# Kernel tuning notes

Measured on AMD Instinct MI355X. Metric: run time of the kernel, lower is better.

Reference implementation:

```python
import jax, jax.numpy as jnp
import numpy as np

NL, DM, DS, DC, EX = 4, 1024, 16, 4, 2
DI = EX * DM          # 2048 inner dim
DTR = DM // 16        # 64 dt_rank
HID, OUT = 2048, 1000
B, L = 2, 1024
EPS = 1e-5

def _ln(x, w, b):
    m = jnp.mean(x, -1, keepdims=True)
    v = jnp.var(x, -1, keepdims=True)
    return (x - m) / jnp.sqrt(v + EPS) * w + b

def _silu(x):
    return x * jax.nn.sigmoid(x)

def _dwconv(x, w, b):
    # x: (B,L,C), w: (C,K) depthwise causal conv
    K = w.shape[1]
    xp = jnp.pad(x, ((0, 0), (K - 1, 0), (0, 0)))
    kern = jnp.transpose(w)[:, None, :]  # (K,1,C)
    y = jax.lax.conv_general_dilated(xp, kern, (1,), 'VALID',
                                     dimension_numbers=('NLC', 'LIO', 'NLC'),
                                     feature_group_count=x.shape[-1])
    return y + b

def _selective_scan(xs_, dt, Bm, Cm, A, Dv):
    # xs_, dt: (B,L,DI); Bm, Cm: (B,L,DS); A: (DI,DS); Dv: (DI,)
    def step(h, inp):
        x_t, dt_t, B_t, C_t = inp  # (B,DI),(B,DI),(B,DS),(B,DS)
        dA = jnp.exp(dt_t[..., None] * A)                       # (B,DI,DS)
        h = dA * h + dt_t[..., None] * B_t[:, None, :] * x_t[..., None]
        return h, jnp.einsum('bdn,bn->bd', h, C_t)
    h0 = jnp.zeros((xs_.shape[0], A.shape[0], A.shape[1]), xs_.dtype)
    seq = tuple(jnp.swapaxes(t, 0, 1) for t in (xs_, dt, Bm, Cm))
    _, ys = jax.lax.scan(step, h0, seq)
    return jnp.swapaxes(ys, 0, 1) + xs_ * Dv

def _mamba_block(x, ipw, cw, cb, xpw, dpw, dpb, Alog, Dv, opw):
    xz = jnp.einsum('bld,ed->ble', x, ipw)          # (B,L,2*DI)
    xs_, z = jnp.split(xz, 2, -1)
    xs_ = _silu(_dwconv(xs_, cw, cb))
    xdbl = jnp.einsum('bld,ed->ble', xs_, xpw)      # (B,L,DTR+2*DS)
    dt, Bm, Cm = jnp.split(xdbl, [DTR, DTR + DS], -1)
    dt = jax.nn.softplus(jnp.einsum('blr,dr->bld', dt, dpw) + dpb)
    A = -jnp.exp(Alog)
    y = _selective_scan(xs_, dt, Bm, Cm, A, Dv)
    y = y * _silu(z)
    return jnp.einsum('bld,ed->ble', y, opw)

def setup_inputs() -> dict:
    key = jax.random.key(0)
    ks = jax.random.split(key, 16)
    s = 0.02
    return {
        'x': jax.random.normal(ks[0], (B, L, DM), jnp.float32),
        'ln_w': jnp.ones((NL, DM)), 'ln_b': jnp.zeros((NL, DM)),
        'in_proj_w': jax.random.normal(ks[1], (NL, 2 * DI, DM)) * s,
        'conv_w': jax.random.normal(ks[2], (NL, DI, DC)) * s,
        'conv_b': jnp.zeros((NL, DI)),
        'x_proj_w': jax.random.normal(ks[3], (NL, DTR + 2 * DS, DI)) * s,
        'dt_proj_w': jax.random.normal(ks[4], (NL, DI, DTR)) * s,
        'dt_proj_b': jax.random.uniform(ks[5], (NL, DI), minval=-4.0, maxval=-2.0),
        'A_log': jnp.log(jnp.broadcast_to(jnp.arange(1, DS + 1, dtype=jnp.float32), (NL, DI, DS)) + 0.0),
        'Dv': jnp.ones((NL, DI)),
        'out_proj_w': jax.random.normal(ks[6], (NL, DM, DI)) * s,
        'fn_w': jnp.ones((DM,)), 'fn_b': jnp.zeros((DM,)),
        'h1_w': jax.random.normal(ks[7], (HID, DM)) * s, 'h1_b': jnp.zeros((HID,)),
        'hln_w': jnp.ones((HID,)), 'hln_b': jnp.zeros((HID,)),
        'h2_w': jax.random.normal(ks[8], (OUT, HID)) * s, 'h2_b': jnp.zeros((OUT,)),
    }

def reference(x, ln_w, ln_b, in_proj_w, conv_w, conv_b, x_proj_w, dt_proj_w,
              dt_proj_b, A_log, Dv, out_proj_w, fn_w, fn_b,
              h1_w, h1_b, hln_w, hln_b, h2_w, h2_b):
    for i in range(NL):
        res = x
        xn = _ln(x, ln_w[i], ln_b[i])
        x = _mamba_block(xn, in_proj_w[i], conv_w[i], conv_b[i], x_proj_w[i],
                         dt_proj_w[i], dt_proj_b[i], A_log[i], Dv[i], out_proj_w[i]) + res
    x = _ln(x, fn_w, fn_b)
    last = x[:, -1, :]                               # (B, DM)
    h = jax.nn.gelu(_ln(last @ h1_w.T + h1_b, hln_w, hln_b), approximate=False)
    return h @ h2_w.T + h2_b                         # (B, OUT)
```

## Files before the change

kernel.cpp:

```cpp
#include <hip/hip_runtime.h>

typedef unsigned short u16;
using short8 = __attribute__((ext_vector_type(8))) short;
using f32x4  = __attribute__((ext_vector_type(4))) float;

#define NLAYER 4
#define DMODEL 1024
#define DSTATE 16
#define DINNER 2048
#define DTRANK 64
#define SEQL   1024
#define NBATCH 2
#define MTOK   2048
#define NCH    64
#define CLEN   16

__device__ __forceinline__ u16 f2bf(float f) {
  union { float f; unsigned int u; } cv; cv.f = f;
  return (u16)((cv.u + 0x7FFFu + ((cv.u >> 16) & 1u)) >> 16);
}
__device__ __forceinline__ float bf2f(u16 v) {
  union { unsigned int u; float f; } cv; cv.u = ((unsigned int)v) << 16; return cv.f;
}

__global__ __launch_bounds__(256) void f32_to_bf16_k(const float* __restrict__ src,
                                                     u16* __restrict__ dst, int n) {
  int i4 = (blockIdx.x * 256 + threadIdx.x) * 4;
  if (i4 >= n) return;
  float4 v = *(const float4*)&src[i4];
  ushort4 o; o.x = f2bf(v.x); o.y = f2bf(v.y); o.z = f2bf(v.z); o.w = f2bf(v.w);
  *(ushort4*)&dst[i4] = o;
}

__global__ __launch_bounds__(256) void cvt_pad_xproj_k(const float* __restrict__ src,
                                                       u16* __restrict__ dst) {
  int i4 = (blockIdx.x * 256 + threadIdx.x) * 4;
  int row = i4 >> 11, col = i4 & 2047;
  float4 v = make_float4(0.f, 0.f, 0.f, 0.f);
  if (row < 96) v = *(const float4*)&src[row * 2048 + col];
  ushort4 o; o.x = f2bf(v.x); o.y = f2bf(v.y); o.z = f2bf(v.z); o.w = f2bf(v.w);
  *(ushort4*)&dst[i4] = o;
}

__global__ __launch_bounds__(256) void cvt_dtin_k(const float* __restrict__ xdbl,
                                                  u16* __restrict__ dtin) {
  int i4 = (blockIdx.x * 256 + threadIdx.x) * 4;
  int m = i4 >> 6, r = i4 & 63;
  float4 v = *(const float4*)&xdbl[m * 128 + r];
  ushort4 o; o.x = f2bf(v.x); o.y = f2bf(v.y); o.z = f2bf(v.z); o.w = f2bf(v.w);
  *(ushort4*)&dtin[i4] = o;
}

__global__ __launch_bounds__(256) void ln_to_bf16_k(const float* __restrict__ X,
    const float* __restrict__ w, const float* __restrict__ b, u16* __restrict__ out) {
  int row = blockIdx.x, tid = threadIdx.x;
  const float* x = X + (size_t)row * 1024;
  float4 v = ((const float4*)x)[tid];
  float s = v.x + v.y + v.z + v.w;
  float q = v.x*v.x + v.y*v.y + v.z*v.z + v.w*v.w;
  for (int o = 32; o; o >>= 1) { s += __shfl_down(s, o); q += __shfl_down(q, o); }
  __shared__ float sb[4], qb[4];
  int wv = tid >> 6, lane = tid & 63;
  if (lane == 0) { sb[wv] = s; qb[wv] = q; }
  __syncthreads();
  s = sb[0] + sb[1] + sb[2] + sb[3];
  q = qb[0] + qb[1] + qb[2] + qb[3];
  float mean = s * (1.f / 1024.f);
  float var  = q * (1.f / 1024.f) - mean * mean;
  float rstd = rsqrtf(var + 1e-5f);
  float4 wv4 = ((const float4*)w)[tid];
  float4 bv4 = ((const float4*)b)[tid];
  ushort4 o4;
  o4.x = f2bf((v.x - mean) * rstd * wv4.x + bv4.x);
  o4.y = f2bf((v.y - mean) * rstd * wv4.y + bv4.y);
  o4.z = f2bf((v.z - mean) * rstd * wv4.z + bv4.z);
  o4.w = f2bf((v.w - mean) * rstd * wv4.w + bv4.w);
  ((ushort4*)(out + (size_t)row * 1024))[tid] = o4;
}

__device__ __forceinline__ void stage_tile(const u16* G, int ld, int row0, int k0,
                                           u16* S, int tid) {
  int w = tid >> 6;
#pragma unroll
  for (int j = 0; j < 2; ++j) {
    int t = tid + j * 256;
    int r = t >> 2;
    int c = (t & 3) << 3;
    const u16* g = G + (size_t)(row0 + r) * ld + (k0 + c);
    u16* s = S + w * 512 + j * 2048;
    __builtin_amdgcn_global_load_lds((const __attribute__((address_space(1))) void*)g,
                                     (__attribute__((address_space(3))) void*)s,
                                     16, 0, 0);
  }
}

template<int EPI>
__global__ __launch_bounds__(256) void gemm_bt(const u16* __restrict__ A,
    const u16* __restrict__ Bw, float* __restrict__ C, const float* __restrict__ bias,
    int lda, int ldb, int ldc, int kchunk) {
  __shared__ u16 As[128 * 32];
  __shared__ u16 Bs[128 * 32];
  int tid = threadIdx.x;
  int bm = blockIdx.x, bn = blockIdx.y;
  int kb = blockIdx.z * kchunk, ke = kb + kchunk;
  int lane = tid & 63, w = tid >> 6;
  int wr = (w >> 1) * 64, wc = (w & 1) * 64;
  int fr = lane & 15;
  int kg = (lane >> 4) * 8;
  f32x4 acc[4][4] = {};
  for (int k0 = kb; k0 < ke; k0 += 32) {
    __syncthreads();
    stage_tile(A, lda, bm * 128, k0, As, tid);
    stage_tile(Bw, ldb, bn * 128, k0, Bs, tid);
    __syncthreads();
    short8 a[4], b[4];
#pragma unroll
    for (int mf = 0; mf < 4; ++mf)
      a[mf] = *(const short8*)&As[(wr + mf * 16 + fr) * 32 + kg];
#pragma unroll
    for (int nf = 0; nf < 4; ++nf)
      b[nf] = *(const short8*)&Bs[(wc + nf * 16 + fr) * 32 + kg];
#pragma unroll
    for (int mf = 0; mf < 4; ++mf)
#pragma unroll
      for (int nf = 0; nf < 4; ++nf)
        acc[mf][nf] = __builtin_amdgcn_mfma_f32_16x16x32_bf16(a[mf], b[nf], acc[mf][nf], 0, 0, 0);
  }
  int r0 = bm * 128 + wr + (lane >> 4) * 4;
  int c0 = bn * 128 + wc + (lane & 15);
#pragma unroll
  for (int mf = 0; mf < 4; ++mf) {
#pragma unroll
    for (int nf = 0; nf < 4; ++nf) {
#pragma unroll
      for (int r = 0; r < 4; ++r) {
        int gr = r0 + mf * 16 + r;
        int gc = c0 + nf * 16;
        float v = acc[mf][nf][r];
        size_t idx = (size_t)gr * ldc + gc;
        if (EPI == 0) {
          C[idx] = v;
        } else if (EPI == 1) {
          ((u16*)C)[idx] = f2bf(v);
        } else if (EPI == 2) {
          v += bias[gc];
          v = (v > 20.f) ? v : log1pf(__expf(v));
          C[idx] = v;
        } else {
          atomicAdd(&C[idx], v);
        }
      }
    }
  }
}

__global__ __launch_bounds__(256) void conv_silu_k(const u16* __restrict__ xzb,
    const float* __restrict__ cw, const float* __restrict__ cb,
    u16* __restrict__ xsb) {
  int idx = blockIdx.x * 256 + threadIdx.x;
  int m = idx >> 9;
  int d = (idx & 511) << 2;
  int t = m & (SEQL - 1);
  float4 w0 = *(const float4*)&cw[(d + 0) * 4];
  float4 w1 = *(const float4*)&cw[(d + 1) * 4];
  float4 w2 = *(const float4*)&cw[(d + 2) * 4];
  float4 w3 = *(const float4*)&cw[(d + 3) * 4];
  float4 acc = *(const float4*)&cb[d];
#pragma unroll
  for (int j = 0; j < 4; ++j) {
    int tt = t - 3 + j;
    if (tt >= 0) {
      ushort4 xv = *(const ushort4*)&xzb[(size_t)(m - 3 + j) * 4096 + d];
      acc.x += bf2f(xv.x) * ((const float*)&w0)[j];
      acc.y += bf2f(xv.y) * ((const float*)&w1)[j];
      acc.z += bf2f(xv.z) * ((const float*)&w2)[j];
      acc.w += bf2f(xv.w) * ((const float*)&w3)[j];
    }
  }
  float4 o;
  o.x = acc.x / (1.f + __expf(-acc.x));
  o.y = acc.y / (1.f + __expf(-acc.y));
  o.z = acc.z / (1.f + __expf(-acc.z));
  o.w = acc.w / (1.f + __expf(-acc.w));
  ushort4 ob; ob.x = f2bf(o.x); ob.y = f2bf(o.y); ob.z = f2bf(o.z); ob.w = f2bf(o.w);
  *(ushort4*)&xsb[(size_t)m * 2048 + d] = ob;
}


__global__ __launch_bounds__(256) void scan_part1(const float* __restrict__ dt,
    const u16* __restrict__ xsb, const float* __restrict__ xdbl,
    const float* __restrict__ Alog, float* __restrict__ PS) {
  int tid = threadIdx.x;
  int dg = blockIdx.x & 7;
  int ch = (blockIdx.x >> 3) & (NCH - 1);
  int b  = blockIdx.x >> 9;
  int d  = dg * 256 + tid;
  float Ar[16];
#pragma unroll
  for (int q = 0; q < 4; ++q) {
    float4 a = *(const float4*)&Alog[d * 16 + q * 4];
    Ar[q*4+0] = -__expf(a.x); Ar[q*4+1] = -__expf(a.y);
    Ar[q*4+2] = -__expf(a.z); Ar[q*4+3] = -__expf(a.w);
  }
  __shared__ float Bs[CLEN][16];
  if (tid < CLEN * 16) {
    int t = tid >> 4, n = tid & 15;
    int m = b * SEQL + ch * CLEN + t;
    Bs[t][n] = xdbl[m * 128 + 64 + n];
  }
  __syncthreads();
  int mbase = b * SEQL + ch * CLEN;
  float dtv[CLEN], xv[CLEN];
#pragma unroll
  for (int t = 0; t < CLEN; ++t) dtv[t] = dt[(size_t)(mbase + t) * 2048 + d];
#pragma unroll
  for (int t = 0; t < CLEN; ++t) xv[t] = bf2f(xsb[(size_t)(mbase + t) * 2048 + d]);
  float S[16];
#pragma unroll
  for (int n = 0; n < 16; ++n) S[n] = 0.f;
  float sumdt = 0.f;
  for (int t = 0; t < CLEN; ++t) {
    sumdt += dtv[t];
    float dx = dtv[t] * xv[t];
    float4 B0 = *(const float4*)&Bs[t][0];
    float4 B1 = *(const float4*)&Bs[t][4];
    float4 B2 = *(const float4*)&Bs[t][8];
    float4 B3 = *(const float4*)&Bs[t][12];
    const float* Bp[4] = {(const float*)&B0, (const float*)&B1, (const float*)&B2, (const float*)&B3};
#pragma unroll
    for (int n = 0; n < 16; ++n)
      S[n] = __expf(dtv[t] * Ar[n]) * S[n] + dx * Bp[n >> 2][n & 3];
  }
  float* p = PS + ((size_t)(b * NCH + ch) * 2048 + d) * 32;
#pragma unroll
  for (int n = 0; n < 16; ++n) p[n] = S[n];
#pragma unroll
  for (int n = 0; n < 16; ++n) p[16 + n] = __expf(Ar[n] * sumdt);
}

__global__ __launch_bounds__(256) void scan_prefix(const float* __restrict__ PS,
                                                   float* __restrict__ Hstart) {
  int id = blockIdx.x * 256 + threadIdx.x;
  int n = id & 15;
  int d = (id >> 4) & 2047;
  int b = id >> 15;
  size_t sbase = ((size_t)b * NCH) * 2048 * 32 + (size_t)d * 32 + n;
  size_t hbase = ((size_t)b * NCH) * 2048 * 16 + (size_t)d * 16 + n;
  float h = 0.f;
#pragma unroll 8
  for (int ch = 0; ch < NCH; ++ch) {
    Hstart[hbase + (size_t)ch * (2048 * 16)] = h;
    float S = PS[sbase + (size_t)ch * (2048 * 32)];
    float P = PS[sbase + (size_t)ch * (2048 * 32) + 16];
    h = fmaf(P, h, S);
  }
}

__global__ __launch_bounds__(256) void scan_part2(const float* __restrict__ dt,
    const u16* __restrict__ xsb, const float* __restrict__ xdbl,
    const float* __restrict__ Alog, const float* __restrict__ Dv,
    const u16* __restrict__ xzb, const float* __restrict__ Hstart,
    u16* __restrict__ yg) {
  int tid = threadIdx.x;
  int dg = blockIdx.x & 7;
  int ch = (blockIdx.x >> 3) & (NCH - 1);
  int b  = blockIdx.x >> 9;
  int d  = dg * 256 + tid;
  float Ar[16];
#pragma unroll
  for (int q = 0; q < 4; ++q) {
    float4 a = *(const float4*)&Alog[d * 16 + q * 4];
    Ar[q*4+0] = -__expf(a.x); Ar[q*4+1] = -__expf(a.y);
    Ar[q*4+2] = -__expf(a.z); Ar[q*4+3] = -__expf(a.w);
  }
  float Dvd = Dv[d];
  __shared__ float BCs[CLEN][32];
  if (tid < 256) {
    int t = tid >> 5, n = tid & 31;
    int m = b * SEQL + ch * CLEN + t;
    BCs[t][n] = xdbl[m * 128 + 64 + n];
    int t2 = t + 8;
    int m2 = m + 8;
    BCs[t2][n] = xdbl[m2 * 128 + 64 + n];
  }
  const float* hs = Hstart + ((size_t)(b * NCH + ch) * 2048 + d) * 16;
  float h[16];
#pragma unroll
  for (int q = 0; q < 4; ++q) {
    float4 hv = *(const float4*)&hs[q * 4];
    h[q*4+0] = hv.x; h[q*4+1] = hv.y; h[q*4+2] = hv.z; h[q*4+3] = hv.w;
  }
  int mbase = b * SEQL + ch * CLEN;
  float dtv[CLEN], xv[CLEN], zv[CLEN];
#pragma unroll
  for (int t = 0; t < CLEN; ++t) dtv[t] = dt[(size_t)(mbase + t) * 2048 + d];
#pragma unroll
  for (int t = 0; t < CLEN; ++t) xv[t] = bf2f(xsb[(size_t)(mbase + t) * 2048 + d]);
#pragma unroll
  for (int t = 0; t < CLEN; ++t) zv[t] = bf2f(xzb[(size_t)(mbase + t) * 4096 + 2048 + d]);
  __syncthreads();
  for (int t = 0; t < CLEN; ++t) {
    float dx = dtv[t] * xv[t];
    float4 B0 = *(const float4*)&BCs[t][0];
    float4 B1 = *(const float4*)&BCs[t][4];
    float4 B2 = *(const float4*)&BCs[t][8];
    float4 B3 = *(const float4*)&BCs[t][12];
    float4 C0 = *(const float4*)&BCs[t][16];
    float4 C1 = *(const float4*)&BCs[t][20];
    float4 C2 = *(const float4*)&BCs[t][24];
    float4 C3 = *(const float4*)&BCs[t][28];
    const float* Bp[4] = {(const float*)&B0, (const float*)&B1, (const float*)&B2, (const float*)&B3};
    const float* Cp[4] = {(const float*)&C0, (const float*)&C1, (const float*)&C2, (const float*)&C3};
#pragma unroll
    for (int n = 0; n < 16; ++n)
      h[n] = __expf(dtv[t] * Ar[n]) * h[n] + dx * Bp[n >> 2][n & 3];
    float y0 = 0.f, y1 = 0.f, y2 = 0.f, y3 = 0.f;
#pragma unroll
    for (int n = 0; n < 4; ++n) {
      y0 += h[n]      * Cp[0][n];
      y1 += h[4 + n]  * Cp[1][n];
      y2 += h[8 + n]  * Cp[2][n];
      y3 += h[12 + n] * Cp[3][n];
    }
    float y = (y0 + y1) + (y2 + y3) + xv[t] * Dvd;
    float sz = zv[t] / (1.f + __expf(-zv[t]));
    yg[(size_t)(mbase + t) * 2048 + d] = f2bf(y * sz);
  }
}

__global__ __launch_bounds__(256) void final_ln_last_k(const float* __restrict__ xb,
    const float* __restrict__ w, const float* __restrict__ b, float* __restrict__ out) {
  int bb = blockIdx.x, tid = threadIdx.x;
  const float* x = xb + (size_t)(bb * 1024 + 1023) * 1024;
  float4 v = ((const float4*)x)[tid];
  float s = v.x + v.y + v.z + v.w;
  float q = v.x*v.x + v.y*v.y + v.z*v.z + v.w*v.w;
  for (int o = 32; o; o >>= 1) { s += __shfl_down(s, o); q += __shfl_down(q, o); }
  __shared__ float sb[4], qb[4];
  int wv = tid >> 6, lane = tid & 63;
  if (lane == 0) { sb[wv] = s; qb[wv] = q; }
  __syncthreads();
  s = sb[0] + sb[1] + sb[2] + sb[3];
  q = qb[0] + qb[1] + qb[2] + qb[3];
  float mean = s * (1.f / 1024.f);
  float rstd = rsqrtf(q * (1.f / 1024.f) - mean * mean + 1e-5f);
  float4 wv4 = ((const float4*)w)[tid];
  float4 bv4 = ((const float4*)b)[tid];
  float4 o;
  o.x = (v.x - mean) * rstd * wv4.x + bv4.x;
  o.y = (v.y - mean) * rstd * wv4.y + bv4.y;
  o.z = (v.z - mean) * rstd * wv4.z + bv4.z;
  o.w = (v.w - mean) * rstd * wv4.w + bv4.w;
  ((float4*)(out + bb * 1024))[tid] = o;
}

__global__ __launch_bounds__(256) void gemv_head1_k(const float* __restrict__ X,
    const float* __restrict__ W, const float* __restrict__ bias, float* __restrict__ out) {
  int gw = (blockIdx.x * 256 + threadIdx.x) >> 6;
  int lane = threadIdx.x & 63;
  int b = gw >> 11, j = gw & 2047;
  const float* x = X + b * 1024;
  const float* w = W + (size_t)j * 1024;
  float s = 0.f;
#pragma unroll
  for (int q = 0; q < 4; ++q) {
    int col = q * 256 + lane * 4;
    float4 xv = *(const float4*)&x[col];
    float4 wv = *(const float4*)&w[col];
    s += xv.x*wv.x + xv.y*wv.y + xv.z*wv.z + xv.w*wv.w;
  }
  for (int o = 32; o; o >>= 1) s += __shfl_down(s, o);
  if (lane == 0) out[gw] = s + bias[j];
}

__global__ __launch_bounds__(256) void ln_gelu_k(const float* __restrict__ X,
    const float* __restrict__ w, const float* __restrict__ b, float* __restrict__ out) {
  int row = blockIdx.x, tid = threadIdx.x;
  const float* x = X + (size_t)row * 2048;
  float4 v0 = ((const float4*)x)[tid];
  float4 v1 = ((const float4*)x)[tid + 256];
  float s = v0.x+v0.y+v0.z+v0.w + v1.x+v1.y+v1.z+v1.w;
  float q = v0.x*v0.x+v0.y*v0.y+v0.z*v0.z+v0.w*v0.w
          + v1.x*v1.x+v1.y*v1.y+v1.z*v1.z+v1.w*v1.w;
  for (int o = 32; o; o >>= 1) { s += __shfl_down(s, o); q += __shfl_down(q, o); }
  __shared__ float sb[4], qb[4];
  int wv = tid >> 6, lane = tid & 63;
  if (lane == 0) { sb[wv] = s; qb[wv] = q; }
  __syncthreads();
  s = sb[0] + sb[1] + sb[2] + sb[3];
  q = qb[0] + qb[1] + qb[2] + qb[3];
  float mean = s * (1.f / 2048.f);
  float rstd = rsqrtf(q * (1.f / 2048.f) - mean * mean + 1e-5f);
  float* o0 = out + (size_t)row * 2048;
#pragma unroll
  for (int h = 0; h < 2; ++h) {
    float4 v = h ? v1 : v0;
    int c0 = tid * 4 + h * 1024;
    float4 wv4 = *(const float4*)&w[c0];
    float4 bv4 = *(const float4*)&b[c0];
    float4 g;
    g.x = (v.x - mean) * rstd * wv4.x + bv4.x;
    g.y = (v.y - mean) * rstd * wv4.y + bv4.y;
    g.z = (v.z - mean) * rstd * wv4.z + bv4.z;
    g.w = (v.w - mean) * rstd * wv4.w + bv4.w;
    g.x = 0.5f * g.x * (1.f + erff(g.x * 0.70710678f));
    g.y = 0.5f * g.y * (1.f + erff(g.y * 0.70710678f));
    g.z = 0.5f * g.z * (1.f + erff(g.z * 0.70710678f));
    g.w = 0.5f * g.w * (1.f + erff(g.w * 0.70710678f));
    *(float4*)&o0[c0] = g;
  }
}

__global__ __launch_bounds__(256) void gemv_head2_k(const float* __restrict__ X,
    const float* __restrict__ W, const float* __restrict__ bias, float* __restrict__ out) {
  int gw = (blockIdx.x * 256 + threadIdx.x) >> 6;
  int lane = threadIdx.x & 63;
  int b = (gw >= 1000) ? 1 : 0;
  int j = gw - b * 1000;
  const float* x = X + b * 2048;
  const float* w = W + (size_t)j * 2048;
  float s = 0.f;
#pragma unroll
  for (int q = 0; q < 8; ++q) {
    int col = q * 256 + lane * 4;
    float4 xv = *(const float4*)&x[col];
    float4 wv = *(const float4*)&w[col];
    s += xv.x*wv.x + xv.y*wv.y + xv.z*wv.z + xv.w*wv.w;
  }
  for (int o = 32; o; o >>= 1) s += __shfl_down(s, o);
  if (lane == 0) out[gw] = s + bias[j];
}

extern "C" void kernel_launch(void* const* d_in, const int* in_sizes, int n_in,
                              void* d_out, int out_size, void* d_ws, size_t ws_size,
                              hipStream_t stream) {
  const float* x_in = (const float*)d_in[0];
  const float* lnw  = (const float*)d_in[1];
  const float* lnb  = (const float*)d_in[2];
  const float* ipw  = (const float*)d_in[3];
  const float* cw   = (const float*)d_in[4];
  const float* cb   = (const float*)d_in[5];
  const float* xpw  = (const float*)d_in[6];
  const float* dpw  = (const float*)d_in[7];
  const float* dpb  = (const float*)d_in[8];
  const float* Alog = (const float*)d_in[9];
  const float* Dv   = (const float*)d_in[10];
  const float* opw  = (const float*)d_in[11];
  const float* fnw  = (const float*)d_in[12];
  const float* fnb  = (const float*)d_in[13];
  const float* h1w  = (const float*)d_in[14];
  const float* h1b  = (const float*)d_in[15];
  const float* hlnw = (const float*)d_in[16];
  const float* hlnb = (const float*)d_in[17];
  const float* h2w  = (const float*)d_in[18];
  const float* h2b  = (const float*)d_in[19];
  float* out = (float*)d_out;

  char* ws = (char*)d_ws;
  size_t off = 0;
  auto alloc = [&](size_t bytes) -> void* {
    void* p = ws + off; off += (bytes + 255) & ~(size_t)255; return p;
  };
  float* x_buf    = (float*)alloc((size_t)MTOK * DMODEL * 4);
  u16*   xn_bf    = (u16*)  alloc((size_t)MTOK * DMODEL * 2);
  u16*   xz_bf    = (u16*)  alloc((size_t)MTOK * 2 * DINNER * 2);
  u16*   xs_bf    = (u16*)  alloc((size_t)MTOK * DINNER * 2);
  float* xdbl     = (float*)alloc((size_t)MTOK * 128 * 4);
  u16*   dtin_bf  = (u16*)  alloc((size_t)MTOK * DTRANK * 2);
  float* dtbuf    = (float*)alloc((size_t)MTOK * DINNER * 4);
  u16*   yg_bf    = (u16*)  alloc((size_t)MTOK * DINNER * 2);
  u16*   w_ip     = (u16*)  alloc((size_t)2 * DINNER * DMODEL * 2);
  u16*   w_xp     = (u16*)  alloc((size_t)128 * DINNER * 2);
  u16*   w_dt     = (u16*)  alloc((size_t)DINNER * DTRANK * 2);
  u16*   w_op     = (u16*)  alloc((size_t)DMODEL * DINNER * 2);
  float* PS       = (float*)alloc((size_t)NBATCH * NCH * DINNER * 32 * 4);
  float* Hstart   = (float*)alloc((size_t)NBATCH * NCH * DINNER * 16 * 4);
  float* lastn    = (float*)alloc(2 * 1024 * 4);
  float* hpre     = (float*)alloc(2 * 2048 * 4);
  float* hbuf     = (float*)alloc(2 * 2048 * 4);

  hipMemcpyAsync(x_buf, x_in, (size_t)MTOK * DMODEL * 4, hipMemcpyDeviceToDevice, stream);

  for (int i = 0; i < NLAYER; ++i) {
    f32_to_bf16_k<<<4096, 256, 0, stream>>>(ipw + (size_t)i * 2 * DINNER * DMODEL, w_ip, 2 * DINNER * DMODEL);
    cvt_pad_xproj_k<<<256, 256, 0, stream>>>(xpw + (size_t)i * 96 * DINNER, w_xp);
    f32_to_bf16_k<<<128, 256, 0, stream>>>(dpw + (size_t)i * DINNER * DTRANK, w_dt, DINNER * DTRANK);
    f32_to_bf16_k<<<2048, 256, 0, stream>>>(opw + (size_t)i * DMODEL * DINNER, w_op, DMODEL * DINNER);
    ln_to_bf16_k<<<MTOK, 256, 0, stream>>>(x_buf, lnw + i * DMODEL, lnb + i * DMODEL, xn_bf);
    { dim3 g(16, 32, 1);
      gemm_bt<1><<<g, 256, 0, stream>>>(xn_bf, w_ip, (float*)xz_bf, nullptr, 1024, 1024, 4096, 1024); }
    conv_silu_k<<<4096, 256, 0, stream>>>(xz_bf, cw + (size_t)i * DINNER * 4, cb + i * DINNER, xs_bf);
    hipMemsetAsync(xdbl, 0, (size_t)MTOK * 128 * 4, stream);
    { dim3 g(16, 1, 8);
      gemm_bt<3><<<g, 256, 0, stream>>>(xs_bf, w_xp, xdbl, nullptr, 2048, 2048, 128, 256); }
    cvt_dtin_k<<<128, 256, 0, stream>>>(xdbl, dtin_bf);
    { dim3 g(16, 16, 1);
      gemm_bt<2><<<g, 256, 0, stream>>>(dtin_bf, w_dt, dtbuf, dpb + i * DINNER, 64, 64, 2048, 64); }
    scan_part1<<<1024, 256, 0, stream>>>(dtbuf, xs_bf, xdbl, Alog + (size_t)i * DINNER * DSTATE, PS);
    scan_prefix<<<256, 256, 0, stream>>>(PS, Hstart);
    scan_part2<<<1024, 256, 0, stream>>>(dtbuf, xs_bf, xdbl, Alog + (size_t)i * DINNER * DSTATE,
                                         Dv + i * DINNER, xz_bf, Hstart, yg_bf);
    { dim3 g(16, 8, 2);
      gemm_bt<3><<<g, 256, 0, stream>>>(yg_bf, w_op, x_buf, nullptr, 2048, 2048, 1024, 1024); }
  }
  final_ln_last_k<<<2, 256, 0, stream>>>(x_buf, fnw, fnb, lastn);
  gemv_head1_k<<<1024, 256, 0, stream>>>(lastn, h1w, h1b, hpre);
  ln_gelu_k<<<2, 256, 0, stream>>>(hpre, hlnw, hlnb, hbuf);
  gemv_head2_k<<<500, 256, 0, stream>>>(hbuf, h2w, h2b, out);
  (void)in_sizes; (void)n_in; (void)out_size; (void)ws_size;
}
```

Before: 800.0 us.

## Fuse conv into x_proj GEMM, double-buffer GEMM, batch weight conversion, bf16 dt

Weight conversion to bf16 now runs once for all layers in batched launches instead of four small launches per layer. The depthwise conv+SiLU is fused into the x_proj GEMM, which also writes xs. The dt-input conversion is fused into a dedicated dt GEMM that stores softplus(dt) as bf16, halving the dt traffic read by both scan kernels. The main GEMM gains LDS double buffering so the next tile loads while MFMA runs on the current one. The cost is more workspace, reduced dt precision, and redundant conv weight loads inside the fused kernel.

```diff
diff --git a/kernel.cpp b/kernel.cpp
--- a/kernel.cpp
+++ b/kernel.cpp
@@ -23,32 +23,25 @@
   union { unsigned int u; float f; } cv; cv.u = ((unsigned int)v) << 16; return cv.f;
 }
 
-__global__ __launch_bounds__(256) void f32_to_bf16_k(const float* __restrict__ src,
-                                                     u16* __restrict__ dst, int n) {
+__global__ __launch_bounds__(256) void f32_to_bf16_l(const float* __restrict__ src,
+                                                     u16* __restrict__ dst, int nper) {
+  int l = blockIdx.y;
   int i4 = (blockIdx.x * 256 + threadIdx.x) * 4;
-  if (i4 >= n) return;
-  float4 v = *(const float4*)&src[i4];
+  if (i4 >= nper) return;
+  float4 v = *(const float4*)&src[(size_t)l * nper + i4];
   ushort4 o; o.x = f2bf(v.x); o.y = f2bf(v.y); o.z = f2bf(v.z); o.w = f2bf(v.w);
-  *(ushort4*)&dst[i4] = o;
-}
-
-__global__ __launch_bounds__(256) void cvt_pad_xproj_k(const float* __restrict__ src,
+  *(ushort4*)&dst[(size_t)l * nper + i4] = o;
+}
+
+__global__ __launch_bounds__(256) void cvt_pad_xproj_l(const float* __restrict__ src,
                                                        u16* __restrict__ dst) {
+  int l = blockIdx.y;
   int i4 = (blockIdx.x * 256 + threadIdx.x) * 4;
   int row = i4 >> 11, col = i4 & 2047;
   float4 v = make_float4(0.f, 0.f, 0.f, 0.f);
-  if (row < 96) v = *(const float4*)&src[row * 2048 + col];
+  if (row < 96) v = *(const float4*)&src[(size_t)l * 96 * 2048 + row * 2048 + col];
   ushort4 o; o.x = f2bf(v.x); o.y = f2bf(v.y); o.z = f2bf(v.z); o.w = f2bf(v.w);
-  *(ushort4*)&dst[i4] = o;
-}
-
-__global__ __launch_bounds__(256) void cvt_dtin_k(const float* __restrict__ xdbl,
-                                                  u16* __restrict__ dtin) {
-  int i4 = (blockIdx.x * 256 + threadIdx.x) * 4;
-  int m = i4 >> 6, r = i4 & 63;
-  float4 v = *(const float4*)&xdbl[m * 128 + r];
-  ushort4 o; o.x = f2bf(v.x); o.y = f2bf(v.y); o.z = f2bf(v.z); o.w = f2bf(v.w);
-  *(ushort4*)&dtin[i4] = o;
+  *(ushort4*)&dst[(size_t)l * 128 * 2048 + i4] = o;
 }
 
 __global__ __launch_bounds__(256) void ln_to_bf16_k(const float* __restrict__ X,
@@ -96,10 +89,10 @@
 
 template<int EPI>
 __global__ __launch_bounds__(256) void gemm_bt(const u16* __restrict__ A,
-    const u16* __restrict__ Bw, float* __restrict__ C, const float* __restrict__ bias,
+    const u16* __restrict__ Bw, float* __restrict__ C,
     int lda, int ldb, int ldc, int kchunk) {
-  __shared__ u16 As[128 * 32];
-  __shared__ u16 Bs[128 * 32];
+  __shared__ u16 As[2][128 * 32];
+  __shared__ u16 Bs[2][128 * 32];
   int tid = threadIdx.x;
   int bm = blockIdx.x, bn = blockIdx.y;
   int kb = blockIdx.z * kchunk, ke = kb + kchunk;
@@ -108,26 +101,33 @@
   int fr = lane & 15;
   int kg = (lane >> 4) * 8;
   f32x4 acc[4][4] = {};
+  int cur = 0;
+  stage_tile(A, lda, bm * 128, kb, As[0], tid);
+  stage_tile(Bw, ldb, bn * 128, kb, Bs[0], tid);
+  __syncthreads();
   for (int k0 = kb; k0 < ke; k0 += 32) {
-    __syncthreads();
-    stage_tile(A, lda, bm * 128, k0, As, tid);
-    stage_tile(Bw, ldb, bn * 128, k0, Bs, tid);
-    __syncthreads();
+    int kn = k0 + 32;
+    if (kn < ke) {
+      stage_tile(A, lda, bm * 128, kn, As[cur ^ 1], tid);
+      stage_tile(Bw, ldb, bn * 128, kn, Bs[cur ^ 1], tid);
+    }
     short8 a[4], b[4];
 #pragma unroll
     for (int mf = 0; mf < 4; ++mf)
-      a[mf] = *(const short8*)&As[(wr + mf * 16 + fr) * 32 + kg];
+      a[mf] = *(const short8*)&As[cur][(wr + mf * 16 + fr) * 32 + kg];
 #pragma unroll
     for (int nf = 0; nf < 4; ++nf)
-      b[nf] = *(const short8*)&Bs[(wc + nf * 16 + fr) * 32 + kg];
+      b[nf] = *(const short8*)&Bs[cur][(wc + nf * 16 + fr) * 32 + kg];
 #pragma unroll
     for (int mf = 0; mf < 4; ++mf)
 #pragma unroll
       for (int nf = 0; nf < 4; ++nf)
         acc[mf][nf] = __builtin_amdgcn_mfma_f32_16x16x32_bf16(a[mf], b[nf], acc[mf][nf], 0, 0, 0);
+    __syncthreads();
+    cur ^= 1;
   }
   int r0 = bm * 128 + wr + (lane >> 4) * 4;
-  int c0 = bn * 128 + wc + (lane & 15);
+  int c0 = bn * 128 + wc + fr;
 #pragma unroll
   for (int mf = 0; mf < 4; ++mf) {
 #pragma unroll
@@ -138,14 +138,8 @@
         int gc = c0 + nf * 16;
         float v = acc[mf][nf][r];
         size_t idx = (size_t)gr * ldc + gc;
-        if (EPI == 0) {
-          C[idx] = v;
-        } else if (EPI == 1) {
+        if (EPI == 1) {
           ((u16*)C)[idx] = f2bf(v);
-        } else if (EPI == 2) {
-          v += bias[gc];
-          v = (v > 20.f) ? v : log1pf(__expf(v));
-          C[idx] = v;
         } else {
           atomicAdd(&C[idx], v);
         }
@@ -154,40 +148,151 @@
   }
 }
 
-__global__ __launch_bounds__(256) void conv_silu_k(const u16* __restrict__ xzb,
+__global__ __launch_bounds__(256) void xproj_conv_k(const u16* __restrict__ xzb,
     const float* __restrict__ cw, const float* __restrict__ cb,
-    u16* __restrict__ xsb) {
-  int idx = blockIdx.x * 256 + threadIdx.x;
-  int m = idx >> 9;
-  int d = (idx & 511) << 2;
-  int t = m & (SEQL - 1);
-  float4 w0 = *(const float4*)&cw[(d + 0) * 4];
-  float4 w1 = *(const float4*)&cw[(d + 1) * 4];
-  float4 w2 = *(const float4*)&cw[(d + 2) * 4];
-  float4 w3 = *(const float4*)&cw[(d + 3) * 4];
-  float4 acc = *(const float4*)&cb[d];
-#pragma unroll
-  for (int j = 0; j < 4; ++j) {
-    int tt = t - 3 + j;
-    if (tt >= 0) {
-      ushort4 xv = *(const ushort4*)&xzb[(size_t)(m - 3 + j) * 4096 + d];
-      acc.x += bf2f(xv.x) * ((const float*)&w0)[j];
-      acc.y += bf2f(xv.y) * ((const float*)&w1)[j];
-      acc.z += bf2f(xv.z) * ((const float*)&w2)[j];
-      acc.w += bf2f(xv.w) * ((const float*)&w3)[j];
+    const u16* __restrict__ Bw, u16* __restrict__ xsb, float* __restrict__ xdbl_l) {
+  __shared__ u16 As[128 * 32];
+  __shared__ u16 Bs[128 * 32];
+  int tid = threadIdx.x;
+  int bm = blockIdx.x;
+  int kb = blockIdx.z * 256;
+  int lane = tid & 63, w = tid >> 6;
+  int wr = (w >> 1) * 64, wc = (w & 1) * 64;
+  int fr = lane & 15;
+  int kg = (lane >> 4) * 8;
+  f32x4 acc[4][4] = {};
+  int r  = tid >> 1;
+  int cc = (tid & 1) * 16;
+  int m  = bm * 128 + r;
+  int tseq = m & (SEQL - 1);
+  for (int k0i = 0; k0i < 256; k0i += 32) {
+    int k0 = kb + k0i;
+    int d0 = k0 + cc;
+    float4 cw4[16];
+#pragma unroll
+    for (int i = 0; i < 16; ++i) cw4[i] = *(const float4*)&cw[(d0 + i) * 4];
+    float accv[16];
+#pragma unroll
+    for (int q = 0; q < 4; ++q) {
+      float4 c4 = *(const float4*)&cb[d0 + q * 4];
+      accv[q*4+0] = c4.x; accv[q*4+1] = c4.y; accv[q*4+2] = c4.z; accv[q*4+3] = c4.w;
     }
-  }
-  float4 o;
-  o.x = acc.x / (1.f + __expf(-acc.x));
-  o.y = acc.y / (1.f + __expf(-acc.y));
-  o.z = acc.z / (1.f + __expf(-acc.z));
-  o.w = acc.w / (1.f + __expf(-acc.w));
-  ushort4 ob; ob.x = f2bf(o.x); ob.y = f2bf(o.y); ob.z = f2bf(o.z); ob.w = f2bf(o.w);
-  *(ushort4*)&xsb[(size_t)m * 2048 + d] = ob;
-}
-
-
-__global__ __launch_bounds__(256) void scan_part1(const float* __restrict__ dt,
+#pragma unroll
+    for (int j = 0; j < 4; ++j) {
+      int tt = tseq - 3 + j;
+      if (tt >= 0) {
+        const u16* src = &xzb[(size_t)(m - 3 + j) * 4096 + d0];
+        short8 v0 = *(const short8*)src;
+        short8 v1 = *(const short8*)(src + 8);
+#pragma unroll
+        for (int i = 0; i < 8; ++i)
+          accv[i] += bf2f((u16)v0[i]) * ((const float*)&cw4[i])[j];
+#pragma unroll
+        for (int i = 0; i < 8; ++i)
+          accv[8 + i] += bf2f((u16)v1[i]) * ((const float*)&cw4[8 + i])[j];
+      }
+    }
+    short8 o0, o1;
+#pragma unroll
+    for (int i = 0; i < 8; ++i) {
+      float s0 = accv[i]     / (1.f + __expf(-accv[i]));
+      float s1 = accv[8 + i] / (1.f + __expf(-accv[8 + i]));
+      o0[i] = (short)f2bf(s0);
+      o1[i] = (short)f2bf(s1);
+    }
+    __syncthreads();
+    *(short8*)&As[r * 32 + cc]     = o0;
+    *(short8*)&As[r * 32 + cc + 8] = o1;
+    stage_tile(Bw, 2048, 0, k0, Bs, tid);
+    *(short8*)&xsb[(size_t)m * 2048 + d0]     = o0;
+    *(short8*)&xsb[(size_t)m * 2048 + d0 + 8] = o1;
+    __syncthreads();
+    short8 a[4], b[4];
+#pragma unroll
+    for (int mf = 0; mf < 4; ++mf)
+      a[mf] = *(const short8*)&As[(wr + mf * 16 + fr) * 32 + kg];
+#pragma unroll
+    for (int nf = 0; nf < 4; ++nf)
+      b[nf] = *(const short8*)&Bs[(wc + nf * 16 + fr) * 32 + kg];
+#pragma unroll
+    for (int mf = 0; mf < 4; ++mf)
+#pragma unroll
+      for (int nf = 0; nf < 4; ++nf)
+        acc[mf][nf] = __builtin_amdgcn_mfma_f32_16x16x32_bf16(a[mf], b[nf], acc[mf][nf], 0, 0, 0);
+  }
+  int r0 = bm * 128 + wr + (lane >> 4) * 4;
+  int c0 = wc + fr;
+#pragma unroll
+  for (int mf = 0; mf < 4; ++mf)
+#pragma unroll
+    for (int nf = 0; nf < 4; ++nf)
+#pragma unroll
+      for (int rr = 0; rr < 4; ++rr) {
+        int gr = r0 + mf * 16 + rr;
+        int gc = c0 + nf * 16;
+        atomicAdd(&xdbl_l[(size_t)gr * 128 + gc], acc[mf][nf][rr]);
+      }
+}
+
+__global__ __launch_bounds__(256) void gemm_dt_k(const float* __restrict__ Af,
+    const u16* __restrict__ Bw, const float* __restrict__ bias, u16* __restrict__ Cout) {
+  __shared__ u16 As[128 * 32];
+  __shared__ u16 Bs[128 * 32];
+  int tid = threadIdx.x;
+  int bm = blockIdx.x, bn = blockIdx.y;
+  int lane = tid & 63, w = tid >> 6;
+  int wr = (w >> 1) * 64, wc = (w & 1) * 64;
+  int fr = lane & 15;
+  int kg = (lane >> 4) * 8;
+  f32x4 acc[4][4] = {};
+  int r  = tid >> 1;
+  int cc = (tid & 1) * 16;
+  for (int k0 = 0; k0 < 64; k0 += 32) {
+    const float* src = &Af[(size_t)(bm * 128 + r) * 128 + k0 + cc];
+    float4 f0 = *(const float4*)&src[0];
+    float4 f1 = *(const float4*)&src[4];
+    float4 f2 = *(const float4*)&src[8];
+    float4 f3 = *(const float4*)&src[12];
+    short8 o0, o1;
+    o0[0]=(short)f2bf(f0.x); o0[1]=(short)f2bf(f0.y); o0[2]=(short)f2bf(f0.z); o0[3]=(short)f2bf(f0.w);
+    o0[4]=(short)f2bf(f1.x); o0[5]=(short)f2bf(f1.y); o0[6]=(short)f2bf(f1.z); o0[7]=(short)f2bf(f1.w);
+    o1[0]=(short)f2bf(f2.x); o1[1]=(short)f2bf(f2.y); o1[2]=(short)f2bf(f2.z); o1[3]=(short)f2bf(f2.w);
+    o1[4]=(short)f2bf(f3.x); o1[5]=(short)f2bf(f3.y); o1[6]=(short)f2bf(f3.z); o1[7]=(short)f2bf(f3.w);
+    __syncthreads();
+    *(short8*)&As[r * 32 + cc]     = o0;
+    *(short8*)&As[r * 32 + cc + 8] = o1;
+    stage_tile(Bw, 64, bn * 128, k0, Bs, tid);
+    __syncthreads();
+    short8 a[4], b[4];
+#pragma unroll
+    for (int mf = 0; mf < 4; ++mf)
+      a[mf] = *(const short8*)&As[(wr + mf * 16 + fr) * 32 + kg];
+#pragma unroll
+    for (int nf = 0; nf < 4; ++nf)
+      b[nf] = *(const short8*)&Bs[(wc + nf * 16 + fr) * 32 + kg];
+#pragma unroll
+    for (int mf = 0; mf < 4; ++mf)
+#pragma unroll
+      for (int nf = 0; nf < 4; ++nf)
+        acc[mf][nf] = __builtin_amdgcn_mfma_f32_16x16x32_bf16(a[mf], b[nf], acc[mf][nf], 0, 0, 0);
+  }
+  int r0 = bm * 128 + wr + (lane >> 4) * 4;
+  int c0 = bn * 128 + wc + fr;
+#pragma unroll
+  for (int mf = 0; mf < 4; ++mf)
+#pragma unroll
+    for (int nf = 0; nf < 4; ++nf)
+#pragma unroll
+      for (int rr = 0; rr < 4; ++rr) {
+        int gr = r0 + mf * 16 + rr;
+        int gc = c0 + nf * 16;
+        float v = acc[mf][nf][rr] + bias[gc];
+        v = (v > 20.f) ? v : log1pf(__expf(v));
+        Cout[(size_t)gr * 2048 + gc] = f2bf(v);
+      }
+}
+
+__global__ __launch_bounds__(256) void scan_part1(const u16* __restrict__ dtb,
     const u16* __restrict__ xsb, const float* __restrict__ xdbl,
     const float* __restrict__ Alog, float* __restrict__ PS) {
   int tid = threadIdx.x;
@@ -202,17 +307,17 @@
     Ar[q*4+0] = -__expf(a.x); Ar[q*4+1] = -__expf(a.y);
     Ar[q*4+2] = -__expf(a.z); Ar[q*4+3] = -__expf(a.w);
   }
-  __shared__ float Bs[CLEN][16];
-  if (tid < CLEN * 16) {
+  __shared__ float Bsh[CLEN][16];
+  {
     int t = tid >> 4, n = tid & 15;
-    int m = b * SEQL + ch * CLEN + t;
-    Bs[t][n] = xdbl[m * 128 + 64 + n];
+    int mm = b * SEQL + ch * CLEN + t;
+    Bsh[t][n] = xdbl[mm * 128 + 64 + n];
   }
   __syncthreads();
   int mbase = b * SEQL + ch * CLEN;
   float dtv[CLEN], xv[CLEN];
 #pragma unroll
-  for (int t = 0; t < CLEN; ++t) dtv[t] = dt[(size_t)(mbase + t) * 2048 + d];
+  for (int t = 0; t < CLEN; ++t) dtv[t] = bf2f(dtb[(size_t)(mbase + t) * 2048 + d]);
 #pragma unroll
   for (int t = 0; t < CLEN; ++t) xv[t] = bf2f(xsb[(size_t)(mbase + t) * 2048 + d]);
   float S[16];
@@ -222,10 +327,10 @@
   for (int t = 0; t < CLEN; ++t) {
     sumdt += dtv[t];
     float dx = dtv[t] * xv[t];
-    float4 B0 = *(const float4*)&Bs[t][0];
-    float4 B1 = *(const float4*)&Bs[t][4];
-    float4 B2 = *(const float4*)&Bs[t][8];
-    float4 B3 = *(const float4*)&Bs[t][12];
+    float4 B0 = *(const float4*)&Bsh[t][0];
+    float4 B1 = *(const float4*)&Bsh[t][4];
+    float4 B2 = *(const float4*)&Bsh[t][8];
+    float4 B3 = *(const float4*)&Bsh[t][12];
     const float* Bp[4] = {(const float*)&B0, (const float*)&B1, (const float*)&B2, (const float*)&B3};
 #pragma unroll
     for (int n = 0; n < 16; ++n)
@@ -256,7 +361,7 @@
   }
 }
 
-__global__ __launch_bounds__(256) void scan_part2(const float* __restrict__ dt,
+__global__ __launch_bounds__(256) void scan_part2(const u16* __restrict__ dtb,
     const u16* __restrict__ xsb, const float* __restrict__ xdbl,
     const float* __restrict__ Alog, const float* __restrict__ Dv,
     const u16* __restrict__ xzb, const float* __restrict__ Hstart,
@@ -275,13 +380,11 @@
   }
   float Dvd = Dv[d];
   __shared__ float BCs[CLEN][32];
-  if (tid < 256) {
+  {
     int t = tid >> 5, n = tid & 31;
-    int m = b * SEQL + ch * CLEN + t;
-    BCs[t][n] = xdbl[m * 128 + 64 + n];
-    int t2 = t + 8;
-    int m2 = m + 8;
-    BCs[t2][n] = xdbl[m2 * 128 + 64 + n];
+    int mm = b * SEQL + ch * CLEN + t;
+    BCs[t][n] = xdbl[mm * 128 + 64 + n];
+    BCs[t + 8][n] = xdbl[(mm + 8) * 128 + 64 + n];
   }
   const float* hs = Hstart + ((size_t)(b * NCH + ch) * 2048 + d) * 16;
   float h[16];
@@ -293,7 +396,7 @@
   int mbase = b * SEQL + ch * CLEN;
   float dtv[CLEN], xv[CLEN], zv[CLEN];
 #pragma unroll
-  for (int t = 0; t < CLEN; ++t) dtv[t] = dt[(size_t)(mbase + t) * 2048 + d];
+  for (int t = 0; t < CLEN; ++t) dtv[t] = bf2f(dtb[(size_t)(mbase + t) * 2048 + d]);
 #pragma unroll
   for (int t = 0; t < CLEN; ++t) xv[t] = bf2f(xsb[(size_t)(mbase + t) * 2048 + d]);
 #pragma unroll
@@ -461,47 +564,49 @@
   auto alloc = [&](size_t bytes) -> void* {
     void* p = ws + off; off += (bytes + 255) & ~(size_t)255; return p;
   };
-  float* x_buf    = (float*)alloc((size_t)MTOK * DMODEL * 4);
-  u16*   xn_bf    = (u16*)  alloc((size_t)MTOK * DMODEL * 2);
-  u16*   xz_bf    = (u16*)  alloc((size_t)MTOK * 2 * DINNER * 2);
-  u16*   xs_bf    = (u16*)  alloc((size_t)MTOK * DINNER * 2);
-  float* xdbl     = (float*)alloc((size_t)MTOK * 128 * 4);
-  u16*   dtin_bf  = (u16*)  alloc((size_t)MTOK * DTRANK * 2);
-  float* dtbuf    = (float*)alloc((size_t)MTOK * DINNER * 4);
-  u16*   yg_bf    = (u16*)  alloc((size_t)MTOK * DINNER * 2);
-  u16*   w_ip     = (u16*)  alloc((size_t)2 * DINNER * DMODEL * 2);
-  u16*   w_xp     = (u16*)  alloc((size_t)128 * DINNER * 2);
-  u16*   w_dt     = (u16*)  alloc((size_t)DINNER * DTRANK * 2);
-  u16*   w_op     = (u16*)  alloc((size_t)DMODEL * DINNER * 2);
-  float* PS       = (float*)alloc((size_t)NBATCH * NCH * DINNER * 32 * 4);
-  float* Hstart   = (float*)alloc((size_t)NBATCH * NCH * DINNER * 16 * 4);
-  float* lastn    = (float*)alloc(2 * 1024 * 4);
-  float* hpre     = (float*)alloc(2 * 2048 * 4);
-  float* hbuf     = (float*)alloc(2 * 2048 * 4);
+  float* x_buf   = (float*)alloc((size_t)MTOK * DMODEL * 4);
+  u16*   xn_bf   = (u16*)  alloc((size_t)MTOK * DMODEL * 2);
+  u16*   xz_bf   = (u16*)  alloc((size_t)MTOK * 2 * DINNER * 2);
+  u16*   xs_bf   = (u16*)  alloc((size_t)MTOK * DINNER * 2);
+  float* xdbl4   = (float*)alloc((size_t)NLAYER * MTOK * 128 * 4);
+  u16*   dtb     = (u16*)  alloc((size_t)MTOK * DINNER * 2);
+  u16*   yg_bf   = (u16*)  alloc((size_t)MTOK * DINNER * 2);
+  u16*   w_ip4   = (u16*)  alloc((size_t)NLAYER * 2 * DINNER * DMODEL * 2);
+  u16*   w_xp4   = (u16*)  alloc((size_t)NLAYER * 128 * DINNER * 2);
+  u16*   w_dt4   = (u16*)  alloc((size_t)NLAYER * DINNER * DTRANK * 2);
+  u16*   w_op4   = (u16*)  alloc((size_t)NLAYER * DMODEL * DINNER * 2);
+  float* PS      = (float*)alloc((size_t)NBATCH * NCH * DINNER * 32 * 4);
+  float* Hstart  = (float*)alloc((size_t)NBATCH * NCH * DINNER * 16 * 4);
+  float* lastn   = (float*)alloc(2 * 1024 * 4);
+  float* hpre    = (float*)alloc(2 * 2048 * 4);
+  float* hbuf    = (float*)alloc(2 * 2048 * 4);
 
   hipMemcpyAsync(x_buf, x_in, (size_t)MTOK * DMODEL * 4, hipMemcpyDeviceToDevice, stream);
+  { dim3 g(4096, 4); f32_to_bf16_l<<<g, 256, 0, stream>>>(ipw, w_ip4, 2 * DINNER * DMODEL); }
+  { dim3 g(256, 4);  cvt_pad_xproj_l<<<g, 256, 0, stream>>>(xpw, w_xp4); }
+  { dim3 g(128, 4);  f32_to_bf16_l<<<g, 256, 0, stream>>>(dpw, w_dt4, DINNER * DTRANK); }
+  { dim3 g(2048, 4); f32_to_bf16_l<<<g, 256, 0, stream>>>(opw, w_op4, DMODEL * DINNER); }
+  hipMemsetAsync(xdbl4, 0, (size_t)NLAYER * MTOK * 128 * 4, stream);
 
   for (int i = 0; i < NLAYER; ++i) {
-    f32_to_bf16_k<<<4096, 256, 0, stream>>>(ipw + (size_t)i * 2 * DINNER * DMODEL, w_ip, 2 * DINNER * DMODEL);
-    cvt_pad_xproj_k<<<256, 256, 0, stream>>>(xpw + (size_t)i * 96 * DINNER, w_xp);
-    f32_to_bf16_k<<<128, 256, 0, stream>>>(dpw + (size_t)i * DINNER * DTRANK, w_dt, DINNER * DTRANK);
-    f32_to_bf16_k<<<2048, 256, 0, stream>>>(opw + (size_t)i * DMODEL * DINNER, w_op, DMODEL * DINNER);
+    float* xdbl_l = xdbl4 + (size_t)i * MTOK * 128;
     ln_to_bf16_k<<<MTOK, 256, 0, stream>>>(x_buf, lnw + i * DMODEL, lnb + i * DMODEL, xn_bf);
     { dim3 g(16, 32, 1);
-      gemm_bt<1><<<g, 256, 0, stream>>>(xn_bf, w_ip, (float*)xz_bf, nullptr, 1024, 1024, 4096, 1024); }
-    conv_silu_k<<<4096, 256, 0, stream>>>(xz_bf, cw + (size_t)i * DINNER * 4, cb + i * DINNER, xs_bf);
-    hipMemsetAsync(xdbl, 0, (size_t)MTOK * 128 * 4, stream);
+      gemm_bt<1><<<g, 256, 0, stream>>>(xn_bf, w_ip4 + (size_t)i * 2 * DINNER * DMODEL,
+                                        (float*)xz_bf, 1024, 1024, 4096, 1024); }
     { dim3 g(16, 1, 8);
-      gemm_bt<3><<<g, 256, 0, stream>>>(xs_bf, w_xp, xdbl, nullptr, 2048, 2048, 128, 256); }
-    cvt_dtin_k<<<128, 256, 0, stream>>>(xdbl, dtin_bf);
+      xproj_conv_k<<<g, 256, 0, stream>>>(xz_bf, cw + (size_t)i * DINNER * 4, cb + i * DINNER,
+                                          w_xp4 + (size_t)i * 128 * DINNER, xs_bf, xdbl_l); }
     { dim3 g(16, 16, 1);
-      gemm_bt<2><<<g, 256, 0, stream>>>(dtin_bf, w_dt, dtbuf, dpb + i * DINNER, 64, 64, 2048, 64); }
-    scan_part1<<<1024, 256, 0, stream>>>(dtbuf, xs_bf, xdbl, Alog + (size_t)i * DINNER * DSTATE, PS);
+      gemm_dt_k<<<g, 256, 0, stream>>>(xdbl_l, w_dt4 + (size_t)i * DINNER * DTRANK,
+                                       dpb + i * DINNER, dtb); }
+    scan_part1<<<1024, 256, 0, stream>>>(dtb, xs_bf, xdbl_l, Alog + (size_t)i * DINNER * DSTATE, PS);
     scan_prefix<<<256, 256, 0, stream>>>(PS, Hstart);
-    scan_part2<<<1024, 256, 0, stream>>>(dtbuf, xs_bf, xdbl, Alog + (size_t)i * DINNER * DSTATE,
+    scan_part2<<<1024, 256, 0, stream>>>(dtb, xs_bf, xdbl_l, Alog + (size_t)i * DINNER * DSTATE,
                                          Dv + i * DINNER, xz_bf, Hstart, yg_bf);
     { dim3 g(16, 8, 2);
-      gemm_bt<3><<<g, 256, 0, stream>>>(yg_bf, w_op, x_buf, nullptr, 2048, 2048, 1024, 1024); }
+      gemm_bt<3><<<g, 256, 0, stream>>>(yg_bf, w_op4 + (size_t)i * DMODEL * DINNER,
+                                        x_buf, 2048, 2048, 1024, 1024); }
   }
   final_ln_last_k<<<2, 256, 0, stream>>>(x_buf, fnw, fnb, lastn);
   gemv_head1_k<<<1024, 256, 0, stream>>>(lastn, h1w, h1b, hpre);
```

Result: faster. 767.2 us (-4.1%).
